# Performance work log

Hardware: AMD Instinct MI355X
Metric: run time of the kernel (lower is better)

## Reference

```python
import jax, jax.numpy as jnp
import numpy as np
from jax import lax

COM, INP, HID, OUT = 128, 512, 2048, 512
T = 16384
SCALE = 35.0  # softmax temperature from the original code


def setup_inputs() -> dict:
    key = jax.random.key(0)
    ks = jax.random.split(key, 10)
    d_in = INP + COM          # 640
    d_out = OUT + COM         # 640
    s1 = 1.0 / np.sqrt(d_in)
    s2 = 1.0 / np.sqrt(HID)
    return {
        "I1": jax.random.normal(ks[0], (T, INP), dtype=jnp.float32),
        "I2": jax.random.normal(ks[1], (T, INP), dtype=jnp.float32),
        "A1W1_w": jax.random.uniform(ks[2], (HID, d_in), jnp.float32, -s1, s1),
        "A1W1_b": jax.random.uniform(ks[3], (HID,), jnp.float32, -s1, s1),
        "A1W2_w": jax.random.uniform(ks[4], (d_out, HID), jnp.float32, -s2, s2),
        "A1W2_b": jax.random.uniform(ks[5], (d_out,), jnp.float32, -s2, s2),
        "A2W1_w": jax.random.uniform(ks[6], (HID, d_in), jnp.float32, -s1, s1),
        "A2W1_b": jax.random.uniform(ks[7], (HID,), jnp.float32, -s1, s1),
        "A2W2_w": jax.random.uniform(ks[8], (d_out, HID), jnp.float32, -s2, s2),
        "A2W2_b": jax.random.uniform(ks[9], (d_out,), jnp.float32, -s2, s2),
    }


def reference(I1, I2, A1W1_w, A1W1_b, A1W2_w, A1W2_b, A2W1_w, A2W1_b, A2W2_w, A2W2_b):
    lrelu = jax.nn.leaky_relu  # negative_slope=0.01, matches torch default
    i1 = I1[0]  # only row 0 is ever used, as in the original forward
    i2 = I2[0]

    def agent1(m2):
        x = jnp.concatenate([i1, m2])
        return lrelu(lrelu(x @ A1W1_w.T + A1W1_b) @ A1W2_w.T + A1W2_b)

    def agent2(m1):
        x = jnp.concatenate([i2, m1])
        return lrelu(lrelu(x @ A2W1_w.T + A2W1_b) @ A2W2_w.T + A2W2_b)

    def step(carry, t):
        sum_c1, sum_c2 = carry  # running sums of com1/com2 rows
        denom = (t + 1).astype(jnp.float32)
        # mean of com2[:t+1]; row t is still zero here (matches torch in-place semantics)
        m2a = sum_c2 / denom
        com1 = jax.nn.softmax(SCALE * agent1(m2a)[OUT:])
        sum_c1 = sum_c1 + com1
        m1 = sum_c1 / denom  # com1[t] now included
        full2 = agent2(m1)
        out2 = full2[:OUT]
        com2 = jax.nn.softmax(SCALE * full2[OUT:])
        sum_c2 = sum_c2 + com2
        m2b = sum_c2 / denom  # com2[t] now included
        out1 = agent1(m2b)[:OUT]
        return (sum_c1, sum_c2), (out1, out2)

    init = (jnp.zeros(COM, jnp.float32), jnp.zeros(COM, jnp.float32))
    _, (out1, out2) = lax.scan(step, init, jnp.arange(I1.shape[0]))
    return out1, out2  # each [T, OUT]
```

## Files before the change

### kernel.cpp

```cpp
#include <hip/hip_runtime.h>
#include <hip/hip_bf16.h>

#define T_STEPS 16384
#define COMD 128
#define INPD 512
#define HIDD 2048
#define OUTD 512
#define DIN 640
#define SCALE_F 35.0f
#define NA 16
#define HSA 128

using u16 = unsigned short;
using u32 = unsigned int;

__device__ __forceinline__ float lrelu(float x){ return x >= 0.f ? x : 0.01f*x; }
__device__ __forceinline__ float bf2f(u16 u){ return __uint_as_float(((u32)u)<<16); }
__device__ __forceinline__ u16 f2bf(float f){ u32 x = __float_as_uint(f); return (u16)((x + 0x7fffu + ((x>>16)&1u)) >> 16); }

__global__ void __launch_bounds__(256) prep_base_kernel(
    const float* __restrict__ I1, const float* __restrict__ I2,
    const float* __restrict__ W11, const float* __restrict__ b11,
    const float* __restrict__ W21, const float* __restrict__ b21,
    float* __restrict__ base)
{
  int row = blockIdx.x*4 + (threadIdx.x>>6);
  int lane = threadIdx.x & 63;
  int agent = row >> 11;
  int h = row & 2047;
  const float* W  = agent ? W21 : W11;
  const float* in = agent ? I2  : I1;
  const float* bv = agent ? b21 : b11;
  float acc = 0.f;
  #pragma unroll
  for (int k = 0; k < 8; ++k)
    acc += W[(size_t)h*DIN + k*64 + lane] * in[k*64 + lane];
  #pragma unroll
  for (int off = 32; off; off >>= 1) acc += __shfl_xor(acc, off);
  if (lane == 0) base[agent*HIDD + h] = acc + bv[h];
}

__global__ void __launch_bounds__(256) cvt_kernel(
    const float* __restrict__ W12, const float* __restrict__ W22,
    u16* __restrict__ o1, u16* __restrict__ o2)
{
  size_t i = ((size_t)blockIdx.x*256 + threadIdx.x)*4;
  float4 a = *reinterpret_cast<const float4*>(W12 + i);
  float4 b = *reinterpret_cast<const float4*>(W22 + i);
  ushort4 ua = { f2bf(a.x), f2bf(a.y), f2bf(a.z), f2bf(a.w) };
  ushort4 ub = { f2bf(b.x), f2bf(b.y), f2bf(b.z), f2bf(b.w) };
  *reinterpret_cast<ushort4*>(o1 + i) = ua;
  *reinterpret_cast<ushort4*>(o2 + i) = ub;
}

__global__ void __launch_bounds__(512, 1) team_kernel(
    const float* __restrict__ W11, const float* __restrict__ W21,
    const float* __restrict__ W12, const float* __restrict__ W22,
    const float* __restrict__ b12, const float* __restrict__ b22,
    const float* __restrict__ base,
    float* __restrict__ P1, float* __restrict__ P2,
    u32* __restrict__ F1, u32* __restrict__ F2,
    void* __restrict__ hist1, void* __restrict__ hist2, int hf32)
{
  __shared__ float sWa[HSA][129];
  __shared__ float sU[COMD][129];
  __shared__ float s_b[HSA], s_st[HSA], s_h[HSA];
  __shared__ float s_bc[COMD], s_com[COMD];
  __shared__ float s_lp[512];

  const int wg = blockIdx.x;
  const bool isA1 = (wg < NA);
  const int g = isA1 ? wg : wg - NA;
  const int h0 = g * HSA;
  const int tid = threadIdx.x;

  const float* W1  = isA1 ? W11 : W21;
  const float* W2  = isA1 ? W12 : W22;
  const float* bL2 = isA1 ? b12 : b22;
  const float* bs  = base + (isA1 ? 0 : HIDD);
  float* Pout = isA1 ? P1 : P2;
  float* Pin  = isA1 ? P2 : P1;
  u32*   Fout = isA1 ? F1 : F2;
  u32*   Fin  = isA1 ? F2 : F1;
  void*  hist = isA1 ? hist1 : hist2;
  float* histf = (float*)hist; u16* histu = (u16*)hist;

  for (int idx = tid; idx < HSA*COMD; idx += 512) {
    int h = idx >> 7, c = idx & 127;
    sWa[h][c] = W1[(size_t)(h0+h)*DIN + INPD + c];
  }
  for (int idx = tid; idx < COMD*HSA; idx += 512) {
    int o = idx >> 7, h = idx & 127;
    sU[o][h] = W2[(size_t)(OUTD+o)*HIDD + h0 + h];
  }
  if (tid < COMD) s_bc[tid] = bL2[OUTD + tid];
  if (tid < HSA) { s_b[tid] = bs[h0 + tid]; s_st[tid] = 0.f; }
  __syncthreads();

  for (int t = 0; t < T_STEPS; ++t) {
    const float invd = 1.f / (float)(t+1);

    if (isA1) {
      if (tid < HSA) s_h[tid] = lrelu(s_b[tid] + s_st[tid]*invd);
      __syncthreads();
      { int o = tid & 127, r = tid >> 7;
        const float* hp = &s_h[r*32];
        float acc = 0.f;
        #pragma unroll
        for (int j = 0; j < 32; ++j) acc += sU[o][r*32+j] * hp[j];
        s_lp[tid] = acc; }
      __syncthreads();
      if (tid < COMD) {
        float p = s_lp[tid]+s_lp[128+tid]+s_lp[256+tid]+s_lp[384+tid];
        __hip_atomic_store(&Pout[g*COMD+tid], p, __ATOMIC_RELAXED, __HIP_MEMORY_SCOPE_AGENT);
      }
      __syncthreads();
      if (tid == 0)
        __hip_atomic_store(&Fout[g*16], (u32)(t+1), __ATOMIC_RELEASE, __HIP_MEMORY_SCOPE_AGENT);
    }

    if (tid < NA) {
      while (__hip_atomic_load(&Fin[tid*16], __ATOMIC_ACQUIRE, __HIP_MEMORY_SCOPE_AGENT) < (u32)(t+1)) {}
    }
    __syncthreads();
    { int o = tid & 127, p4 = tid >> 7;
      float s = 0.f;
      #pragma unroll
      for (int j = 0; j < 4; ++j)
        s += __hip_atomic_load(&Pin[(p4*4+j)*COMD + o], __ATOMIC_RELAXED, __HIP_MEMORY_SCOPE_AGENT);
      s_lp[tid] = s; }
    __syncthreads();
    if (tid < 64) {
      int o0 = tid, o1 = tid + 64;
      float z0 = SCALE_F * lrelu(s_lp[o0]+s_lp[128+o0]+s_lp[256+o0]+s_lp[384+o0] + s_bc[o0]);
      float z1 = SCALE_F * lrelu(s_lp[o1]+s_lp[128+o1]+s_lp[256+o1]+s_lp[384+o1] + s_bc[o1]);
      float m = fmaxf(z0, z1);
      #pragma unroll
      for (int off = 32; off; off >>= 1) m = fmaxf(m, __shfl_xor(m, off));
      float e0 = __expf(z0 - m), e1 = __expf(z1 - m);
      float s = e0 + e1;
      #pragma unroll
      for (int off = 32; off; off >>= 1) s += __shfl_xor(s, off);
      float r = 1.f / s;
      s_com[o0] = e0 * r; s_com[o1] = e1 * r;
    }
    __syncthreads();
    { int h = tid & 127, q = tid >> 7;
      const float* cp = &s_com[q*32];
      float acc = 0.f;
      #pragma unroll
      for (int j = 0; j < 32; ++j) acc += sWa[h][q*32+j] * cp[j];
      s_lp[tid] = acc; }
    __syncthreads();
    if (tid < HSA) {
      float st = s_st[tid] + s_lp[tid]+s_lp[128+tid]+s_lp[256+tid]+s_lp[384+tid];
      s_st[tid] = st;
      float x = lrelu(s_b[tid] + st*invd);
      s_h[tid] = x;
      if (hf32) histf[(size_t)t*HIDD + h0 + tid] = x;
      else      histu[(size_t)t*HIDD + h0 + tid] = f2bf(x);
    }

    if (!isA1) {
      __syncthreads();
      { int o = tid & 127, r = tid >> 7;
        const float* hp = &s_h[r*32];
        float acc = 0.f;
        #pragma unroll
        for (int j = 0; j < 32; ++j) acc += sU[o][r*32+j] * hp[j];
        s_lp[tid] = acc; }
      __syncthreads();
      if (tid < COMD) {
        float p = s_lp[tid]+s_lp[128+tid]+s_lp[256+tid]+s_lp[384+tid];
        __hip_atomic_store(&Pout[g*COMD+tid], p, __ATOMIC_RELAXED, __HIP_MEMORY_SCOPE_AGENT);
      }
      __syncthreads();
      if (tid == 0)
        __hip_atomic_store(&Fout[g*16], (u32)(t+1), __ATOMIC_RELEASE, __HIP_MEMORY_SCOPE_AGENT);
    }
  }
}

__global__ void __launch_bounds__(256) out_kernel(
    const void* __restrict__ hist1, const void* __restrict__ hist2,
    const u16* __restrict__ Wb1, const u16* __restrict__ Wb2,
    const float* __restrict__ b12, const float* __restrict__ b22,
    float* __restrict__ out, int hf32)
{
  __shared__ float hl[8][2048];
  const int head = blockIdx.x & 1;
  const int t0 = (blockIdx.x >> 1) * 8;
  const int tid = threadIdx.x;
  const void* hist = head ? hist2 : hist1;
  const u16* W = head ? Wb2 : Wb1;
  const float* bias = head ? b22 : b12;
  float* op = out + (size_t)head * T_STEPS * OUTD;

  if (hf32) {
    const float* hf = (const float*)hist;
    for (int idx = tid; idx < 8*2048; idx += 256)
      hl[idx>>11][idx&2047] = hf[(size_t)t0*HIDD + idx];
  } else {
    const u16* hu = (const u16*)hist;
    for (int idx = tid; idx < 8*2048; idx += 256)
      hl[idx>>11][idx&2047] = bf2f(hu[(size_t)t0*HIDD + idx]);
  }
  __syncthreads();

  const int wave = tid >> 6, lane = tid & 63;
  for (int row = wave; row < OUTD; row += 4) {
    const u16* wr = W + (size_t)row*HIDD;
    float acc[8] = {0,0,0,0,0,0,0,0};
    #pragma unroll
    for (int k = 0; k < 8; ++k) {
      const int e = k*256 + lane*4;
      uint2 pw = *reinterpret_cast<const uint2*>(wr + e);
      float w0 = bf2f((u16)(pw.x & 0xffffu));
      float w1 = bf2f((u16)(pw.x >> 16));
      float w2 = bf2f((u16)(pw.y & 0xffffu));
      float w3 = bf2f((u16)(pw.y >> 16));
      #pragma unroll
      for (int tt = 0; tt < 8; ++tt) {
        const float4 hv = *reinterpret_cast<const float4*>(&hl[tt][e]);
        acc[tt] += w0*hv.x + w1*hv.y + w2*hv.z + w3*hv.w;
      }
    }
    #pragma unroll
    for (int tt = 0; tt < 8; ++tt) {
      float a = acc[tt];
      #pragma unroll
      for (int off = 32; off; off >>= 1) a += __shfl_xor(a, off);
      acc[tt] = a;
    }
    if (lane == 0) {
      const float b = bias[row];
      #pragma unroll
      for (int tt = 0; tt < 8; ++tt)
        op[(size_t)(t0+tt)*OUTD + row] = lrelu(acc[tt] + b);
    }
  }
}

extern "C" void kernel_launch(void* const* d_in, const int* in_sizes, int n_in,
                              void* d_out, int out_size, void* d_ws, size_t ws_size,
                              hipStream_t stream)
{
  const float* I1  = (const float*)d_in[0];
  const float* I2  = (const float*)d_in[1];
  const float* W11 = (const float*)d_in[2];
  const float* b11 = (const float*)d_in[3];
  const float* W12 = (const float*)d_in[4];
  const float* b12 = (const float*)d_in[5];
  const float* W21 = (const float*)d_in[6];
  const float* b21 = (const float*)d_in[7];
  const float* W22 = (const float*)d_in[8];
  const float* b22 = (const float*)d_in[9];

  char* ws = (char*)d_ws;
  float* base = (float*)ws;
  float* P1 = (float*)(ws + 16384);
  float* P2 = (float*)(ws + 32768);
  u32* F1 = (u32*)(ws + 49152);
  u32* F2 = (u32*)(ws + 53248);
  char* hist1 = ws + 65536;
  const size_t histF = (size_t)T_STEPS*HIDD*4;
  const size_t histU = (size_t)T_STEPS*HIDD*2;
  const size_t wbB   = (size_t)OUTD*HIDD*2;
  const size_t needF = 65536 + 2*histF + 2*wbB;
  int hf32 = (ws_size >= needF) ? 1 : 0;
  const size_t hb = hf32 ? histF : histU;
  char* hist2 = hist1 + hb;
  u16* Wb1 = (u16*)(hist2 + hb);
  u16* Wb2 = Wb1 + (size_t)OUTD*HIDD;

  hipMemsetAsync(ws + 49152, 0, 8192, stream);
  prep_base_kernel<<<1024, 256, 0, stream>>>(I1, I2, W11, b11, W21, b21, base);
  cvt_kernel<<<1024, 256, 0, stream>>>(W12, W22, Wb1, Wb2);

  void* h1v = (void*)hist1; void* h2v = (void*)hist2;
  void* kargs[] = { (void*)&W11, (void*)&W21, (void*)&W12, (void*)&W22,
                    (void*)&b12, (void*)&b22, (void*)&base,
                    (void*)&P1, (void*)&P2, (void*)&F1, (void*)&F2,
                    (void*)&h1v, (void*)&h2v, (void*)&hf32 };
  hipLaunchCooperativeKernel((const void*)team_kernel, dim3(2*NA), dim3(512),
                             kargs, 0, stream);

  out_kernel<<<(T_STEPS/8)*2, 256, 0, stream>>>(h1v, h2v, Wb1, Wb2, b12, b22,
                                                (float*)d_out, hf32);
}
```

Before: 121.7 ms.

## Use single-wave workgroups and tag-embedded partials to replace flag synchronization

The persistent team kernel shrinks each workgroup from 512 threads to a single 64-lane wavefront, so most __syncthreads barriers and the cross-thread partial-sum reductions in LDS go away; each lane now computes two full 128-long dot products. The separate release/acquire flag is removed. Instead, a 2-bit step tag is packed into the low mantissa bits of each partial sum, and consumers spin with relaxed loads until every tag matches. This cuts one round trip of inter-workgroup latency per handoff on the serial critical path, in exchange for a slight precision loss in the partials, longer per-lane dot loops, and reliance on relaxed-atomic ordering.

```diff
diff --git a/kernel.cpp b/kernel.cpp
--- a/kernel.cpp
+++ b/kernel.cpp
@@ -17,6 +17,9 @@
 __device__ __forceinline__ float lrelu(float x){ return x >= 0.f ? x : 0.01f*x; }
 __device__ __forceinline__ float bf2f(u16 u){ return __uint_as_float(((u32)u)<<16); }
 __device__ __forceinline__ u16 f2bf(float f){ u32 x = __float_as_uint(f); return (u16)((x + 0x7fffu + ((x>>16)&1u)) >> 16); }
+__device__ __forceinline__ u32 aload(const u32* p){ return __hip_atomic_load(p, __ATOMIC_RELAXED, __HIP_MEMORY_SCOPE_AGENT); }
+__device__ __forceinline__ void astore(u32* p, u32 v){ __hip_atomic_store(p, v, __ATOMIC_RELAXED, __HIP_MEMORY_SCOPE_AGENT); }
+__device__ __forceinline__ u32 tagf(float f, u32 tg){ return (__float_as_uint(f) & ~3u) | tg; }
 
 __global__ void __launch_bounds__(256) prep_base_kernel(
     const float* __restrict__ I1, const float* __restrict__ I2,
@@ -53,87 +56,89 @@
   *reinterpret_cast<ushort4*>(o2 + i) = ub;
 }
 
-__global__ void __launch_bounds__(512, 1) team_kernel(
+__global__ void __launch_bounds__(64, 1) team_kernel(
     const float* __restrict__ W11, const float* __restrict__ W21,
     const float* __restrict__ W12, const float* __restrict__ W22,
     const float* __restrict__ b12, const float* __restrict__ b22,
     const float* __restrict__ base,
-    float* __restrict__ P1, float* __restrict__ P2,
-    u32* __restrict__ F1, u32* __restrict__ F2,
+    u32* __restrict__ P1, u32* __restrict__ P2,
     void* __restrict__ hist1, void* __restrict__ hist2, int hf32)
 {
-  __shared__ float sWa[HSA][129];
-  __shared__ float sU[COMD][129];
-  __shared__ float s_b[HSA], s_st[HSA], s_h[HSA];
-  __shared__ float s_bc[COMD], s_com[COMD];
-  __shared__ float s_lp[512];
+  __shared__ float sWa[HSA*129];
+  __shared__ float sU[COMD*129];
+  __shared__ float s_h[HSA];
+  __shared__ float s_com[COMD];
 
   const int wg = blockIdx.x;
   const bool isA1 = (wg < NA);
   const int g = isA1 ? wg : wg - NA;
   const int h0 = g * HSA;
-  const int tid = threadIdx.x;
-
-  const float* W1  = isA1 ? W11 : W21;
-  const float* W2  = isA1 ? W12 : W22;
-  const float* bL2 = isA1 ? b12 : b22;
-  const float* bs  = base + (isA1 ? 0 : HIDD);
-  float* Pout = isA1 ? P1 : P2;
-  float* Pin  = isA1 ? P2 : P1;
-  u32*   Fout = isA1 ? F1 : F2;
-  u32*   Fin  = isA1 ? F2 : F1;
-  void*  hist = isA1 ? hist1 : hist2;
+  const int l = threadIdx.x;
+
+  const float* W1 = isA1 ? W11 : W21;
+  const float* W2 = isA1 ? W12 : W22;
+  const float* bOth = isA1 ? b22 : b12;
+  u32* Pout = isA1 ? P1 : P2;
+  u32* Pin  = isA1 ? P2 : P1;
+  void* hist = isA1 ? hist1 : hist2;
   float* histf = (float*)hist; u16* histu = (u16*)hist;
 
-  for (int idx = tid; idx < HSA*COMD; idx += 512) {
-    int h = idx >> 7, c = idx & 127;
-    sWa[h][c] = W1[(size_t)(h0+h)*DIN + INPD + c];
-  }
-  for (int idx = tid; idx < COMD*HSA; idx += 512) {
-    int o = idx >> 7, h = idx & 127;
-    sU[o][h] = W2[(size_t)(OUTD+o)*HIDD + h0 + h];
-  }
-  if (tid < COMD) s_bc[tid] = bL2[OUTD + tid];
-  if (tid < HSA) { s_b[tid] = bs[h0 + tid]; s_st[tid] = 0.f; }
+  for (int idx = l; idx < HSA*COMD; idx += 64) {
+    int r = idx >> 7, c = idx & 127;
+    sWa[r*129+c] = W1[(size_t)(h0+r)*DIN + INPD + c];
+    sU [r*129+c] = W2[(size_t)(OUTD+r)*HIDD + h0 + c];
+  }
+  const float bc0 = bOth[OUTD + l];
+  const float bc1 = bOth[OUTD + 64 + l];
+  const float sb0 = base[(isA1?0:HIDD) + h0 + l];
+  const float sb1 = base[(isA1?0:HIDD) + h0 + 64 + l];
+  float st0 = 0.f, st1 = 0.f;
   __syncthreads();
 
   for (int t = 0; t < T_STEPS; ++t) {
     const float invd = 1.f / (float)(t+1);
-
-    if (isA1) {
-      if (tid < HSA) s_h[tid] = lrelu(s_b[tid] + s_st[tid]*invd);
+    const u32 tg = (u32)((t+1) & 3);
+
+    auto produce = [&]() {
+      float x0 = lrelu(sb0 + st0*invd);
+      float x1 = lrelu(sb1 + st1*invd);
+      s_h[l] = x0; s_h[64+l] = x1;
       __syncthreads();
-      { int o = tid & 127, r = tid >> 7;
-        const float* hp = &s_h[r*32];
-        float acc = 0.f;
+      float p0 = 0.f, p1 = 0.f;
+      #pragma unroll 16
+      for (int h = 0; h < HSA; ++h) {
+        float hv = s_h[h];
+        p0 += sU[l*129+h]*hv;
+        p1 += sU[(64+l)*129+h]*hv;
+      }
+      astore(&Pout[g*COMD + l],      tagf(p0, tg));
+      astore(&Pout[g*COMD + 64 + l], tagf(p1, tg));
+    };
+
+    if (isA1) produce();
+
+    {
+      u32 v0[NA], v1[NA];
+      for (;;) {
         #pragma unroll
-        for (int j = 0; j < 32; ++j) acc += sU[o][r*32+j] * hp[j];
-        s_lp[tid] = acc; }
-      __syncthreads();
-      if (tid < COMD) {
-        float p = s_lp[tid]+s_lp[128+tid]+s_lp[256+tid]+s_lp[384+tid];
-        __hip_atomic_store(&Pout[g*COMD+tid], p, __ATOMIC_RELAXED, __HIP_MEMORY_SCOPE_AGENT);
-      }
-      __syncthreads();
-      if (tid == 0)
-        __hip_atomic_store(&Fout[g*16], (u32)(t+1), __ATOMIC_RELEASE, __HIP_MEMORY_SCOPE_AGENT);
-    }
-
-    if (tid < NA) {
-      while (__hip_atomic_load(&Fin[tid*16], __ATOMIC_ACQUIRE, __HIP_MEMORY_SCOPE_AGENT) < (u32)(t+1)) {}
-    }
-    __syncthreads();
-    { int o = tid & 127, p4 = tid >> 7;
-      float s = 0.f;
-      #pragma unroll
-      for (int j = 0; j < 4; ++j)
-        s += __hip_atomic_load(&Pin[(p4*4+j)*COMD + o], __ATOMIC_RELAXED, __HIP_MEMORY_SCOPE_AGENT);
-      s_lp[tid] = s; }
-    __syncthreads();
-    if (tid < 64) {
-      int o0 = tid, o1 = tid + 64;
-      float z0 = SCALE_F * lrelu(s_lp[o0]+s_lp[128+o0]+s_lp[256+o0]+s_lp[384+o0] + s_bc[o0]);
-      float z1 = SCALE_F * lrelu(s_lp[o1]+s_lp[128+o1]+s_lp[256+o1]+s_lp[384+o1] + s_bc[o1]);
+        for (int j = 0; j < NA; ++j) v0[j] = aload(&Pin[j*COMD + l]);
+        #pragma unroll
+        for (int j = 0; j < NA; ++j) v1[j] = aload(&Pin[j*COMD + 64 + l]);
+        u32 bad = 0;
+        #pragma unroll
+        for (int j = 0; j < NA; ++j)
+          bad |= ((v0[j]&3u)^tg) | ((v1[j]&3u)^tg);
+        if (!bad) break;
+        __builtin_amdgcn_s_sleep(1);
+      }
+      float z0 = bc0, z1 = bc1;
+      #pragma unroll
+      for (int j = 0; j < NA; ++j) {
+        z0 += __uint_as_float(v0[j] & ~3u);
+        z1 += __uint_as_float(v1[j] & ~3u);
+      }
+      z0 = SCALE_F * lrelu(z0);
+      z1 = SCALE_F * lrelu(z1);
       float m = fmaxf(z0, z1);
       #pragma unroll
       for (int off = 32; off; off >>= 1) m = fmaxf(m, __shfl_xor(m, off));
@@ -141,43 +146,29 @@
       float s = e0 + e1;
       #pragma unroll
       for (int off = 32; off; off >>= 1) s += __shfl_xor(s, off);
-      float r = 1.f / s;
-      s_com[o0] = e0 * r; s_com[o1] = e1 * r;
-    }
-    __syncthreads();
-    { int h = tid & 127, q = tid >> 7;
-      const float* cp = &s_com[q*32];
-      float acc = 0.f;
-      #pragma unroll
-      for (int j = 0; j < 32; ++j) acc += sWa[h][q*32+j] * cp[j];
-      s_lp[tid] = acc; }
-    __syncthreads();
-    if (tid < HSA) {
-      float st = s_st[tid] + s_lp[tid]+s_lp[128+tid]+s_lp[256+tid]+s_lp[384+tid];
-      s_st[tid] = st;
-      float x = lrelu(s_b[tid] + st*invd);
-      s_h[tid] = x;
-      if (hf32) histf[(size_t)t*HIDD + h0 + tid] = x;
-      else      histu[(size_t)t*HIDD + h0 + tid] = f2bf(x);
-    }
-
-    if (!isA1) {
+      float rs = 1.f / s;
+      s_com[l] = e0 * rs; s_com[64+l] = e1 * rs;
       __syncthreads();
-      { int o = tid & 127, r = tid >> 7;
-        const float* hp = &s_h[r*32];
-        float acc = 0.f;
-        #pragma unroll
-        for (int j = 0; j < 32; ++j) acc += sU[o][r*32+j] * hp[j];
-        s_lp[tid] = acc; }
-      __syncthreads();
-      if (tid < COMD) {
-        float p = s_lp[tid]+s_lp[128+tid]+s_lp[256+tid]+s_lp[384+tid];
-        __hip_atomic_store(&Pout[g*COMD+tid], p, __ATOMIC_RELAXED, __HIP_MEMORY_SCOPE_AGENT);
-      }
-      __syncthreads();
-      if (tid == 0)
-        __hip_atomic_store(&Fout[g*16], (u32)(t+1), __ATOMIC_RELEASE, __HIP_MEMORY_SCOPE_AGENT);
-    }
+      float a0 = 0.f, a1 = 0.f;
+      #pragma unroll 16
+      for (int c = 0; c < COMD; ++c) {
+        float cv = s_com[c];
+        a0 += sWa[l*129+c]*cv;
+        a1 += sWa[(64+l)*129+c]*cv;
+      }
+      st0 += a0; st1 += a1;
+      float x0 = lrelu(sb0 + st0*invd);
+      float x1 = lrelu(sb1 + st1*invd);
+      if (hf32) {
+        histf[(size_t)t*HIDD + h0 + l]      = x0;
+        histf[(size_t)t*HIDD + h0 + 64 + l] = x1;
+      } else {
+        histu[(size_t)t*HIDD + h0 + l]      = f2bf(x0);
+        histu[(size_t)t*HIDD + h0 + 64 + l] = f2bf(x1);
+      }
+    }
+
+    if (!isA1) produce();
   }
 }
 
@@ -258,10 +249,8 @@
 
   char* ws = (char*)d_ws;
   float* base = (float*)ws;
-  float* P1 = (float*)(ws + 16384);
-  float* P2 = (float*)(ws + 32768);
-  u32* F1 = (u32*)(ws + 49152);
-  u32* F2 = (u32*)(ws + 53248);
+  u32* P1 = (u32*)(ws + 16384);
+  u32* P2 = (u32*)(ws + 24576);
   char* hist1 = ws + 65536;
   const size_t histF = (size_t)T_STEPS*HIDD*4;
   const size_t histU = (size_t)T_STEPS*HIDD*2;
@@ -273,16 +262,16 @@
   u16* Wb1 = (u16*)(hist2 + hb);
   u16* Wb2 = Wb1 + (size_t)OUTD*HIDD;
 
-  hipMemsetAsync(ws + 49152, 0, 8192, stream);
+  hipMemsetAsync(ws + 16384, 0, 16384, stream);
   prep_base_kernel<<<1024, 256, 0, stream>>>(I1, I2, W11, b11, W21, b21, base);
   cvt_kernel<<<1024, 256, 0, stream>>>(W12, W22, Wb1, Wb2);
 
   void* h1v = (void*)hist1; void* h2v = (void*)hist2;
   void* kargs[] = { (void*)&W11, (void*)&W21, (void*)&W12, (void*)&W22,
                     (void*)&b12, (void*)&b22, (void*)&base,
-                    (void*)&P1, (void*)&P2, (void*)&F1, (void*)&F2,
+                    (void*)&P1, (void*)&P2,
                     (void*)&h1v, (void*)&h2v, (void*)&hf32 };
-  hipLaunchCooperativeKernel((const void*)team_kernel, dim3(2*NA), dim3(512),
+  hipLaunchCooperativeKernel((const void*)team_kernel, dim3(2*NA), dim3(64),
                              kargs, 0, stream);
 
   out_kernel<<<(T_STEPS/8)*2, 256, 0, stream>>>(h1v, h2v, Wb1, Wb2, b12, b22,
```

Result: slower. 158.5 ms (+30.2%).
